# Kernel tuning notes

Hardware: AMD Instinct MI355X
Metric: run time of the kernel (lower is better)

Reference implementation:

```python
import jax, jax.numpy as jnp
import numpy as np

B, S, E, H, W = 2, 4096, 1024, 8, 8  # batch, seq, embed, heads, window


def build_window_idx(seq_len):
    """Replicates the original Python loop EXACTLY, including the bug where
    relative offsets in [-4,3] are used directly as (negatively-wrapping)
    absolute indices."""
    rows = []
    for t in range(seq_len):
        rp = [i for i in range(-4, 4) if 0 <= t + i < seq_len]
        while len(rp) < 8:
            if t + len(rp) < seq_len:
                rp.append(t + len(rp))
            else:
                rp.insert(0, t - (8 - len(rp)))
        rows.append([p % seq_len for p in rp])  # python negative indexing
    return np.asarray(rows, dtype=np.int32)  # [S, 8]


def setup_inputs() -> dict:
    key = jax.random.key(0)
    ks = jax.random.split(key, 7)
    return {
        "q": jax.random.normal(ks[0], (B, S, E), jnp.float32),
        "k": jax.random.normal(ks[1], (B, S, E), jnp.float32),
        "v": jax.random.normal(ks[2], (B, S, E), jnp.float32),
        "in_proj_w": jax.random.normal(ks[3], (3 * E, E), jnp.float32) * 0.02,
        "in_proj_b": jax.random.normal(ks[4], (3 * E,), jnp.float32) * 0.02,
        "out_w": jax.random.normal(ks[5], (E, E), jnp.float32) * 0.02,
        "out_b": jax.random.normal(ks[6], (E,), jnp.float32) * 0.02,
    }


def reference(q, k, v, in_proj_w, in_proj_b, out_w, out_b):
    b, s, e = q.shape
    d = e // H
    scale = 1.0 / np.sqrt(d).astype(np.float32)
    idx = jnp.asarray(build_window_idx(s))  # [S, 8] static gather indices

    Wq, Wk, Wv = in_proj_w[:e], in_proj_w[e:2 * e], in_proj_w[2 * e:]
    bq, bk, bv = in_proj_b[:e], in_proj_b[e:2 * e], in_proj_b[2 * e:]

    kg = k[:, idx]  # [B, S, 8, E] gathered key windows
    vg = v[:, idx]  # [B, S, 8, E]

    qh = (q @ Wq.T + bq).reshape(b, s, H, d)          # [B,S,H,D]
    kh = (kg @ Wk.T + bk).reshape(b, s, W, H, d)      # [B,S,8,H,D]
    vh = (vg @ Wv.T + bv).reshape(b, s, W, H, d)      # [B,S,8,H,D]

    scores = jnp.einsum('bshd,bswhd->bshw', qh * scale, kh)  # [B,S,H,8]
    attn = jax.nn.softmax(scores, axis=-1)  # dropout inactive (eval mode)
    o = jnp.einsum('bshw,bswhd->bshd', attn, vh).reshape(b, s, e)
    return o @ out_w.T + out_b  # [B, S, E]
```

## Files before the change

### kernel.cpp

```cpp
#include <hip/hip_runtime.h>
#include <hip/hip_bf16.h>
#include <math.h>

#define SEQ   4096
#define EMB   1024
#define NH    8
#define HD    128
#define NSLOT 15

typedef __attribute__((ext_vector_type(8))) short bf16x8;
typedef __attribute__((ext_vector_type(4))) float f32x4;
typedef __attribute__((ext_vector_type(4))) unsigned short ushort4v;
typedef unsigned short ushort_t;

__device__ __constant__ unsigned int MULT[8] = {
    0x00005555u,
    0x10015055u,
    0x14050055u,
    0x15100055u,
    0x15800015u,
    0x16800005u,
    0x1A800001u,
    0x15400055u
};

__device__ __forceinline__ unsigned short f2bf(float x) {
    unsigned int u = __float_as_uint(x);
    return (unsigned short)((u + 0x7FFFu + ((u >> 16) & 1u)) >> 16);
}

__device__ __forceinline__ bf16x8 cvt8(float4 a, float4 b) {
    union { unsigned int u[4]; bf16x8 v; } r;
    asm("v_cvt_pk_bf16_f32 %0, %1, %2" : "=v"(r.u[0]) : "v"(a.x), "v"(a.y));
    asm("v_cvt_pk_bf16_f32 %0, %1, %2" : "=v"(r.u[1]) : "v"(a.z), "v"(a.w));
    asm("v_cvt_pk_bf16_f32 %0, %1, %2" : "=v"(r.u[2]) : "v"(b.x), "v"(b.y));
    asm("v_cvt_pk_bf16_f32 %0, %1, %2" : "=v"(r.u[3]) : "v"(b.z), "v"(b.w));
    return r.v;
}

__device__ __forceinline__ int xcd_swz(int bid, int nwg) {
    int cpx = nwg >> 3;
    return (bid & 7) * cpx + (bid >> 3);
}

__global__ __launch_bounds__(256) void proj_kv_small(
    const float* __restrict__ k, const float* __restrict__ v,
    const float* __restrict__ ipw, const float* __restrict__ ipb,
    float* __restrict__ kvp) {
    int fc  = blockIdx.x & 63;
    int bkv = blockIdx.x >> 6;
    int kv  = bkv & 1;
    int b   = bkv >> 1;

    const float* x0 = (kv ? v : k) + (size_t)b * SEQ * EMB;
    const float* Wm = ipw + (size_t)(1 + kv) * EMB * EMB;
    const float* bb = ipb + (size_t)(1 + kv) * EMB;

    __shared__ __align__(16) float xs[NSLOT][EMB + 4];
    int tid = threadIdx.x;
#pragma unroll
    for (int i = 0; i < NSLOT; i++) {
        int pos = (i < 11) ? i : (SEQ - 4 + (i - 11));
        *(float4*)&xs[i][tid * 4] = *(const float4*)&x0[(size_t)pos * EMB + tid * 4];
    }
    __syncthreads();

    int row  = tid & 15;
    int feat = fc * 16 + (tid >> 4);
    if (row < NSLOT) {
        const float* wrow = Wm + (size_t)feat * EMB;
        float acc0 = 0.f, acc1 = 0.f;
#pragma unroll 4
        for (int kk = 0; kk < EMB; kk += 8) {
            float4 xv0 = *(const float4*)&xs[row][kk];
            float4 wv0 = *(const float4*)&wrow[kk];
            float4 xv1 = *(const float4*)&xs[row][kk + 4];
            float4 wv1 = *(const float4*)&wrow[kk + 4];
            acc0 += xv0.x * wv0.x + xv0.y * wv0.y + xv0.z * wv0.z + xv0.w * wv0.w;
            acc1 += xv1.x * wv1.x + xv1.y * wv1.y + xv1.z * wv1.z + xv1.w * wv1.w;
        }
        kvp[((size_t)((b * 2 + kv) * NSLOT + row)) * EMB + feat] = acc0 + acc1 + bb[feat];
    }
}

union GUShared {
    struct { float xs[HD]; float red[HD]; } gm;
    float vs[NSLOT][256 + 4];
};
__global__ __launch_bounds__(256) void gu_pre(
    const float* __restrict__ kvp, const float* __restrict__ ipw,
    const float* __restrict__ ipb, const float* __restrict__ outw,
    ushort_t* __restrict__ G, float* __restrict__ cvec,
    ushort_t* __restrict__ UT, int nGm) {
    __shared__ __align__(16) GUShared sm;
    int tid = threadIdx.x;

    if (blockIdx.x < (unsigned)nGm) {
        int hs = blockIdx.x & 127, b = blockIdx.x >> 7;
        int h = hs >> 4, s = hs & 15;
        if (tid < HD)
            sm.gm.xs[tid] = (s < NSLOT)
                ? kvp[((size_t)((b * 2 + 0) * NSLOT + s)) * EMB + h * HD + tid] : 0.f;
        __syncthreads();
        int e0 = tid * 4;
        float a0 = 0.f, a1 = 0.f, a2 = 0.f, a3 = 0.f;
#pragma unroll 8
        for (int d = 0; d < HD; d++) {
            float xv = sm.gm.xs[d];
            const float* wr_ = ipw + (size_t)(h * HD + d) * EMB + e0;
            a0 += xv * wr_[0]; a1 += xv * wr_[1]; a2 += xv * wr_[2]; a3 += xv * wr_[3];
        }
        ushort4v gv; gv[0] = f2bf(a0); gv[1] = f2bf(a1); gv[2] = f2bf(a2); gv[3] = f2bf(a3);
        int kc = e0 >> 3;
        *(ushort4v*)&G[(size_t)b * 131072 + kc * 1024 + hs * 8 + (e0 & 7)] = gv;

        if (tid < HD) sm.gm.red[tid] = sm.gm.xs[tid] * ipb[h * HD + tid];
        __syncthreads();
        if (tid < 64) {
            float vsum = sm.gm.red[tid] + sm.gm.red[tid + 64];
            vsum += __shfl_down(vsum, 32, 64); vsum += __shfl_down(vsum, 16, 64);
            vsum += __shfl_down(vsum, 8, 64);  vsum += __shfl_down(vsum, 4, 64);
            vsum += __shfl_down(vsum, 2, 64);  vsum += __shfl_down(vsum, 1, 64);
            if (tid == 0) cvec[b * 128 + hs] = vsum;
        }
    } else {
        int idx = blockIdx.x - nGm;
        int ec = idx & 63;
        int hp = (idx >> 6) & 3;
        int b  = idx >> 8;
        for (int i = tid; i < NSLOT * 64; i += 256) {
            int s_ = i >> 6, j4 = i & 63;
            *(float4*)&sm.vs[s_][j4 * 4] = *(const float4*)
                &kvp[((size_t)((b * 2 + 1) * NSLOT + s_)) * EMB + hp * 256 + j4 * 4];
        }
        __syncthreads();
        int s = tid & 15, el = tid >> 4;
        int e = ec * 16 + el;
#pragma unroll
        for (int hh = 0; hh < 2; hh++) {
            int h = hp * 2 + hh;
            float acc0 = 0.f, acc1 = 0.f;
            if (s < NSLOT) {
                const float* orow = outw + (size_t)e * EMB + h * HD;
                const float* vrow = &sm.vs[s][hh * 128];
#pragma unroll 4
                for (int d = 0; d < HD; d += 8) {
                    float4 o0 = *(const float4*)&orow[d];
                    float4 v0 = *(const float4*)&vrow[d];
                    float4 o1 = *(const float4*)&orow[d + 4];
                    float4 v1 = *(const float4*)&vrow[d + 4];
                    acc0 += o0.x * v0.x + o0.y * v0.y + o0.z * v0.z + o0.w * v0.w;
                    acc1 += o1.x * v1.x + o1.y * v1.y + o1.z * v1.z + o1.w * v1.w;
                }
            }
            int hs = h * 16 + s;
            UT[(size_t)b * 131072 + (hs >> 3) * 8192 + e * 8 + (hs & 7)]
                = f2bf(acc0 + acc1);
        }
    }
}

#define TBM 16
#define NTQ 8
__global__ __launch_bounds__(512) void score_out(
    const float* __restrict__ q, const ushort_t* __restrict__ G,
    const float* __restrict__ cvec, const ushort_t* __restrict__ UT,
    const float* __restrict__ outb, float* __restrict__ out) {
    __shared__ __align__(16) union {
        ushort_t qbf[TBM * 1024];
        ushort_t pl[TBM * 128];
    } sm;

    int tid = threadIdx.x, lane = tid & 63, w = tid >> 6;
    int fr = lane & 15, g = lane >> 4;
    int lb  = xcd_swz(blockIdx.x, gridDim.x);
    int mb0 = lb * TBM;
    int b   = mb0 >> 12;

    const ushort_t* Gb = G + (size_t)b * 131072;
    int hsb = w * 16;
    float cv = cvec[b * 128 + hsb + fr];

#pragma unroll
    for (int r = 0; r < 2; r++) {
        int row = w * 2 + r;
        const float* qrp = q + (size_t)(mb0 + row) * EMB;
#pragma unroll
        for (int c = 0; c < 2; c++) {
            int k0 = c * 512 + lane * 8;
            float4 x0 = *(const float4*)(qrp + k0);
            float4 x1 = *(const float4*)(qrp + k0 + 4);
            bf16x8 vv = cvt8(x0, x1);
            int gi = k0 >> 3;
            int gs_ = (gi & ~15) | ((gi & 15) ^ row);
            *(bf16x8*)&sm.qbf[row * 1024 + gs_ * 8] = vv;
        }
    }
    __syncthreads();

    f32x4 acc0 = {}, acc1 = {};
#pragma unroll
    for (int t = 0; t < NTQ; t += 2) {
        __builtin_amdgcn_s_setprio(1);
#pragma unroll
        for (int sub = 0; sub < 4; sub++) {
            int gi0 = t * 16 + ((sub * 4 + g) ^ fr);
            bf16x8 af0 = *(const bf16x8*)&sm.qbf[fr * 1024 + gi0 * 8];
            int kc0 = t * 16 + sub * 4 + g;
            bf16x8 bf0 = *(const bf16x8*)&Gb[((size_t)kc0 * 128 + hsb + fr) * 8];
            acc0 = __builtin_amdgcn_mfma_f32_16x16x32_bf16(af0, bf0, acc0, 0, 0, 0);
            int gi1 = (t + 1) * 16 + ((sub * 4 + g) ^ fr);
            bf16x8 af1 = *(const bf16x8*)&sm.qbf[fr * 1024 + gi1 * 8];
            int kc1 = (t + 1) * 16 + sub * 4 + g;
            bf16x8 bf1 = *(const bf16x8*)&Gb[((size_t)kc1 * 128 + hsb + fr) * 8];
            acc1 = __builtin_amdgcn_mfma_f32_16x16x32_bf16(af1, bf1, acc1, 0, 0, 0);
        }
        __builtin_amdgcn_s_setprio(0);
    }
    f32x4 acc = acc0 + acc1;

    __syncthreads();

    const float scale = 0.08838834764831845f;
#pragma unroll
    for (int r = 0; r < 4; r++) {
        int row = g * 4 + r;
        int tl  = (mb0 + row) & (SEQ - 1);
        int cse = (tl >= 4 && tl <= SEQ - 4) ? 7 : ((tl < 4) ? tl : tl - (SEQ - 3) + 4);
        float mult = (float)((MULT[cse] >> (fr * 2)) & 3u);
        float vv = (acc[r] + cv) * scale;
        float vm = (mult != 0.f) ? vv : -1e30f;
#pragma unroll
        for (int sh = 1; sh < 16; sh <<= 1) vm = fmaxf(vm, __shfl_xor(vm, sh, 64));
        float e_ = mult * expf(vv - vm);
        float z = e_;
#pragma unroll
        for (int sh = 1; sh < 16; sh <<= 1) z += __shfl_xor(z, sh, 64);
        int col = hsb + fr;
        int cg  = col >> 3;
        int pg  = (cg & 8) | ((cg & 7) ^ (row & 7));
        sm.pl[row * 128 + pg * 8 + (col & 7)] = f2bf(e_ / z);
    }
    __syncthreads();

    const ushort_t* UTb = UT + (size_t)b * 131072;
    int eb = w * 128;
#pragma unroll
    for (int n = 0; n < 8; n++) {
        int e = eb + n * 16 + fr;
        f32x4 o2 = {};
#pragma unroll
        for (int kk = 0; kk < 4; kk++) {
            int gi = kk * 4 + g;
            bf16x8 ub = *(const bf16x8*)&UTb[((size_t)gi * 1024 + e) * 8];
            int pg = (gi & 8) | ((gi & 7) ^ (fr & 7));
            bf16x8 pa = *(const bf16x8*)&sm.pl[fr * 128 + pg * 8];
            o2 = __builtin_amdgcn_mfma_f32_16x16x32_bf16(pa, ub, o2, 0, 0, 0);
        }
        float bn = outb[e];
#pragma unroll
        for (int r = 0; r < 4; r++)
            out[(size_t)(mb0 + g * 4 + r) * EMB + e] = o2[r] + bn;
    }
}

extern "C" void kernel_launch(void* const* d_in, const int* in_sizes, int n_in,
                              void* d_out, int out_size, void* d_ws, size_t ws_size,
                              hipStream_t stream) {
    const float* q    = (const float*)d_in[0];
    const float* k    = (const float*)d_in[1];
    const float* v    = (const float*)d_in[2];
    const float* ipw  = (const float*)d_in[3];
    const float* ipb  = (const float*)d_in[4];
    const float* outw = (const float*)d_in[5];
    const float* outb = (const float*)d_in[6];
    float* out = (float*)d_out;

    int Bb = in_sizes[0] / (SEQ * EMB);
    int M  = Bb * SEQ;

    float*    kvp  = (float*)d_ws;
    ushort_t* G    = (ushort_t*)(kvp + (size_t)Bb * 2 * NSLOT * EMB);
    ushort_t* UTm  = G + (size_t)Bb * 131072;
    float*    cvec = (float*)(UTm + (size_t)Bb * 131072);

    proj_kv_small<<<dim3(Bb * 2 * 64), dim3(256), 0, stream>>>(k, v, ipw, ipb, kvp);
    gu_pre<<<dim3(Bb * 128 + Bb * 256), dim3(256), 0, stream>>>(
        kvp, ipw, ipb, outw, G, cvec, UTm, Bb * 128);
    score_out<<<dim3(M / TBM), dim3(512), 0, stream>>>(q, G, cvec, UTm, outb, out);
}
```

Measured before the change: 54.11 us.

## Split score GEMM K-dimension across two wave groups with 1024-thread blocks

```diff
diff --git a/kernel.cpp b/kernel.cpp
--- a/kernel.cpp
+++ b/kernel.cpp
@@ -161,92 +161,97 @@
 }
 
 #define TBM 16
-#define NTQ 8
-__global__ __launch_bounds__(512) void score_out(
+__global__ __launch_bounds__(1024) void score_out(
     const float* __restrict__ q, const ushort_t* __restrict__ G,
     const float* __restrict__ cvec, const ushort_t* __restrict__ UT,
     const float* __restrict__ outb, float* __restrict__ out) {
-    __shared__ __align__(16) union {
-        ushort_t qbf[TBM * 1024];
-        ushort_t pl[TBM * 128];
-    } sm;
+    __shared__ __align__(16) ushort_t qbf[TBM * 1024];
+    __shared__ __align__(16) float part[4096];
+    __shared__ __align__(16) ushort_t pl[TBM * 128];
 
     int tid = threadIdx.x, lane = tid & 63, w = tid >> 6;
+    int h = w & 7, khalf = w >> 3;
     int fr = lane & 15, g = lane >> 4;
     int lb  = xcd_swz(blockIdx.x, gridDim.x);
     int mb0 = lb * TBM;
     int b   = mb0 >> 12;
 
     const ushort_t* Gb = G + (size_t)b * 131072;
-    int hsb = w * 16;
-    float cv = cvec[b * 128 + hsb + fr];
-
-#pragma unroll
-    for (int r = 0; r < 2; r++) {
-        int row = w * 2 + r;
+    int hsb = h * 16;
+
+#pragma unroll
+    for (int c = 0; c < 2; c++) {
+        int row = w;
         const float* qrp = q + (size_t)(mb0 + row) * EMB;
-#pragma unroll
-        for (int c = 0; c < 2; c++) {
-            int k0 = c * 512 + lane * 8;
-            float4 x0 = *(const float4*)(qrp + k0);
-            float4 x1 = *(const float4*)(qrp + k0 + 4);
-            bf16x8 vv = cvt8(x0, x1);
-            int gi = k0 >> 3;
-            int gs_ = (gi & ~15) | ((gi & 15) ^ row);
-            *(bf16x8*)&sm.qbf[row * 1024 + gs_ * 8] = vv;
-        }
+        int k0 = c * 512 + lane * 8;
+        float4 x0 = *(const float4*)(qrp + k0);
+        float4 x1 = *(const float4*)(qrp + k0 + 4);
+        bf16x8 vv = cvt8(x0, x1);
+        int gi = k0 >> 3;
+        int gs_ = (gi & ~15) | ((gi & 15) ^ row);
+        *(bf16x8*)&qbf[row * 1024 + gs_ * 8] = vv;
     }
     __syncthreads();
 
     f32x4 acc0 = {}, acc1 = {};
-#pragma unroll
-    for (int t = 0; t < NTQ; t += 2) {
+    int tbase = khalf * 4;
+#pragma unroll
+    for (int t = 0; t < 4; t += 2) {
         __builtin_amdgcn_s_setprio(1);
 #pragma unroll
         for (int sub = 0; sub < 4; sub++) {
-            int gi0 = t * 16 + ((sub * 4 + g) ^ fr);
-            bf16x8 af0 = *(const bf16x8*)&sm.qbf[fr * 1024 + gi0 * 8];
-            int kc0 = t * 16 + sub * 4 + g;
+            int gi0 = (tbase + t) * 16 + ((sub * 4 + g) ^ fr);
+            bf16x8 af0 = *(const bf16x8*)&qbf[fr * 1024 + gi0 * 8];
+            int kc0 = (tbase + t) * 16 + sub * 4 + g;
             bf16x8 bf0 = *(const bf16x8*)&Gb[((size_t)kc0 * 128 + hsb + fr) * 8];
             acc0 = __builtin_amdgcn_mfma_f32_16x16x32_bf16(af0, bf0, acc0, 0, 0, 0);
-            int gi1 = (t + 1) * 16 + ((sub * 4 + g) ^ fr);
-            bf16x8 af1 = *(const bf16x8*)&sm.qbf[fr * 1024 + gi1 * 8];
-            int kc1 = (t + 1) * 16 + sub * 4 + g;
+            int gi1 = (tbase + t + 1) * 16 + ((sub * 4 + g) ^ fr);
+            bf16x8 af1 = *(const bf16x8*)&qbf[fr * 1024 + gi1 * 8];
+            int kc1 = (tbase + t + 1) * 16 + sub * 4 + g;
             bf16x8 bf1 = *(const bf16x8*)&Gb[((size_t)kc1 * 128 + hsb + fr) * 8];
             acc1 = __builtin_amdgcn_mfma_f32_16x16x32_bf16(af1, bf1, acc1, 0, 0, 0);
         }
         __builtin_amdgcn_s_setprio(0);
     }
-    f32x4 acc = acc0 + acc1;
-
-    __syncthreads();
-
-    const float scale = 0.08838834764831845f;
+    f32x4 accp = acc0 + acc1;
 #pragma unroll
     for (int r = 0; r < 4; r++) {
         int row = g * 4 + r;
-        int tl  = (mb0 + row) & (SEQ - 1);
-        int cse = (tl >= 4 && tl <= SEQ - 4) ? 7 : ((tl < 4) ? tl : tl - (SEQ - 3) + 4);
-        float mult = (float)((MULT[cse] >> (fr * 2)) & 3u);
-        float vv = (acc[r] + cv) * scale;
-        float vm = (mult != 0.f) ? vv : -1e30f;
-#pragma unroll
-        for (int sh = 1; sh < 16; sh <<= 1) vm = fmaxf(vm, __shfl_xor(vm, sh, 64));
-        float e_ = mult * expf(vv - vm);
-        float z = e_;
-#pragma unroll
-        for (int sh = 1; sh < 16; sh <<= 1) z += __shfl_xor(z, sh, 64);
-        int col = hsb + fr;
-        int cg  = col >> 3;
-        int pg  = (cg & 8) | ((cg & 7) ^ (row & 7));
-        sm.pl[row * 128 + pg * 8 + (col & 7)] = f2bf(e_ / z);
+        part[((khalf * 8 + h) * 16 + row) * 16 + fr] = accp[r];
+    }
+    __syncthreads();
+
+    if (khalf == 0) {
+        float cv = cvec[b * 128 + hsb + fr];
+        const float scale = 0.08838834764831845f;
+#pragma unroll
+        for (int r = 0; r < 4; r++) {
+            int row = g * 4 + r;
+            float sc = part[(h * 16 + row) * 16 + fr]
+                     + part[((8 + h) * 16 + row) * 16 + fr];
+            int tl  = (mb0 + row) & (SEQ - 1);
+            int cse = (tl >= 4 && tl <= SEQ - 4) ? 7 : ((tl < 4) ? tl : tl - (SEQ - 3) + 4);
+            float mult = (float)((MULT[cse] >> (fr * 2)) & 3u);
+            float vv = (sc + cv) * scale;
+            float vm = (mult != 0.f) ? vv : -1e30f;
+#pragma unroll
+            for (int sh = 1; sh < 16; sh <<= 1) vm = fmaxf(vm, __shfl_xor(vm, sh, 64));
+            float e_ = mult * expf(vv - vm);
+            float z = e_;
+#pragma unroll
+            for (int sh = 1; sh < 16; sh <<= 1) z += __shfl_xor(z, sh, 64);
+            int col = hsb + fr;
+            int cg  = col >> 3;
+            int pg  = (cg & 8) | ((cg & 7) ^ (row & 7));
+            pl[row * 128 + pg * 8 + (col & 7)] = f2bf(e_ / z);
+        }
     }
     __syncthreads();
 
     const ushort_t* UTb = UT + (size_t)b * 131072;
-    int eb = w * 128;
-#pragma unroll
-    for (int n = 0; n < 8; n++) {
+    int eb = h * 128 + khalf * 64;
+#pragma unroll
+    for (int n = 0; n < 4; n++) {
         int e = eb + n * 16 + fr;
         f32x4 o2 = {};
 #pragma unroll
@@ -254,7 +259,7 @@
             int gi = kk * 4 + g;
             bf16x8 ub = *(const bf16x8*)&UTb[((size_t)gi * 1024 + e) * 8];
             int pg = (gi & 8) | ((gi & 7) ^ (fr & 7));
-            bf16x8 pa = *(const bf16x8*)&sm.pl[fr * 128 + pg * 8];
+            bf16x8 pa = *(const bf16x8*)&pl[fr * 128 + pg * 8];
             o2 = __builtin_amdgcn_mfma_f32_16x16x32_bf16(pa, ub, o2, 0, 0, 0);
         }
         float bn = outb[e];
@@ -287,5 +292,5 @@
     proj_kv_small<<<dim3(Bb * 2 * 64), dim3(256), 0, stream>>>(k, v, ipw, ipb, kvp);
     gu_pre<<<dim3(Bb * 128 + Bb * 256), dim3(256), 0, stream>>>(
         kvp, ipw, ipb, outw, G, cvec, UTm, Bb * 128);
-    score_out<<<dim3(M / TBM), dim3(512), 0, stream>>>(q, G, cvec, UTm, outb, out);
-}
+    score_out<<<dim3(M / TBM), dim3(1024), 0, stream>>>(q, G, cvec, UTm, outb, out);
+}
```

Result: slower. 57.27 us (+5.8%).
